# Optimization experiments

Measured on AMD Instinct MI355X. Metric: run time of the kernel, lower is better.

## Reference

```python
import jax, jax.numpy as jnp
import numpy as np
import math

B = 1024
FV = 4096
E = 256
Z = E + 1
EPS = 1e-3
INNER_NSTEP = 8
INNER_LR = 0.5
NS = 16


def setup_inputs() -> dict:
    key = jax.random.key(0)
    ks = jax.random.split(key, 6)
    img = jax.random.uniform(ks[0], (B, FV), dtype=jnp.float32)
    lab = jax.random.randint(ks[1], (B,), 0, 10, dtype=jnp.int64)
    w_dec_w = jax.random.normal(ks[2], (FV, E), dtype=jnp.float32) / np.sqrt(E)
    w_dec_b = jnp.zeros((FV,), dtype=jnp.float32)
    whz_w = jax.random.normal(ks[3], (E, Z), dtype=jnp.float32) / np.sqrt(Z)
    whz_b = jnp.zeros((E,), dtype=jnp.float32)
    b_loc_prior = jax.random.normal(ks[4], (Z,), dtype=jnp.float32) * 0.1
    b_scale_out = jnp.zeros((), dtype=jnp.float32)
    return {"img": img, "lab": lab, "w_dec_w": w_dec_w, "w_dec_b": w_dec_b,
            "whz_w": whz_w, "whz_b": whz_b, "b_loc_prior": b_loc_prior,
            "b_scale_out": b_scale_out}


def reference(img, lab, w_dec_w, w_dec_b, whz_w, whz_b, b_loc_prior, b_scale_out):
    del lab  # unused by loss_joint_lp
    img_flat = img.reshape((img.shape[0], -1))  # [B, FV]
    Bn = img_flat.shape[0]
    node_h = jnp.full((Bn, E), EPS, dtype=img.dtype)
    node_z = jnp.full((Bn, Z), EPS, dtype=img.dtype)
    out_prec = jnp.exp(2.0 * b_scale_out)
    log_prior_sig = jax.nn.log_sigmoid(b_loc_prior)  # [Z]

    def step(carry, k):
        node_h, node_z = carry
        k1, k2 = jax.random.split(k)
        node_e = node_h @ w_dec_w.T + w_dec_b                     # [B, FV]
        dh1 = ((img_flat - node_e) * out_prec) @ w_dec_w          # [B, E]
        h_post_log = node_z @ whz_w.T + whz_b                     # [B, E]
        dh2 = jax.nn.log_sigmoid(h_post_log)
        dz1 = (node_h * jax.nn.sigmoid(-h_post_log)) @ whz_w + log_prior_sig  # [B, Z]
        h_next = jax.nn.sigmoid(dh1 + dh2)
        z_next = jax.nn.sigmoid(dz1)
        sel_h = jax.random.uniform(k1, node_h.shape) < INNER_LR
        sel_z = jax.random.uniform(k2, node_z.shape) < INNER_LR
        node_h = jnp.where(sel_h, 0.5 * (node_h + h_next), node_h)
        node_z = jnp.where(sel_z, 0.5 * (node_z + z_next), node_z)
        node_h = jax.lax.stop_gradient(node_h)  # mirrors .detach()
        node_z = jax.lax.stop_gradient(node_z)
        return (node_h, node_z), None

    loop_keys = jax.random.split(jax.random.key(42), INNER_NSTEP)
    (node_h, node_z), _ = jax.lax.scan(step, (node_h, node_z), loop_keys)

    # Importance-weighted bound with NS Bernoulli samples
    sk = jax.random.split(jax.random.key(7), 2)
    z_noise = (jax.random.uniform(sk[0], (NS, Bn, Z)) < node_z).astype(img.dtype)
    h_post_log = z_noise @ whz_w.T + whz_b                        # [NS, B, E]
    h_noise = (jax.random.uniform(sk[1], (NS, Bn, E)) < jax.nn.sigmoid(h_post_log)).astype(img.dtype)
    loc = h_noise @ w_dec_w.T + w_dec_b                           # [NS, B, FV]

    # Normal(loc, exp(b_scale_out)).log_prob(img_flat)
    inv_scale = jnp.exp(-b_scale_out)
    lp_external = (-0.5 * ((img_flat - loc) * inv_scale) ** 2
                   - b_scale_out - 0.5 * math.log(2.0 * math.pi))  # [NS, B, FV]

    # Bernoulli(logits=b_loc_prior).log_prob - Bernoulli(probs=node_z).log_prob
    lp_prior = z_noise * b_loc_prior - jax.nn.softplus(b_loc_prior)
    lp_post = z_noise * jnp.log(node_z) + (1.0 - z_noise) * jnp.log1p(-node_z)
    lp_internal = lp_prior - lp_post                               # [NS, B, Z]

    joint = lp_internal.sum(-1) + lp_external.sum(-1)              # [NS, B]
    lse = jax.nn.logsumexp(joint, axis=0) - math.log(NS)           # [B]
    return -lse.mean(0)
```

## Files before the change

### kernel.cpp

```cpp
#include <hip/hip_runtime.h>
#include <stdint.h>

#define B_    1024
#define FV_   4096
#define E_    256
#define Z_    257
#define NS_   16
#define NSB_  16384
#define EPS_  1e-3f

typedef __attribute__((ext_vector_type(8))) short short8v;
typedef __attribute__((ext_vector_type(4))) float f32x4;
#define MFMA16(a,b,c) __builtin_amdgcn_mfma_f32_16x16x32_bf16(a,b,c,0,0,0)

__host__ __device__ __forceinline__ uint32_t rotl32(uint32_t v, int r){
  return (v << r) | (v >> (32 - r));
}
__host__ __device__ __forceinline__ void tf2x32(uint32_t k0, uint32_t k1,
    uint32_t x0, uint32_t x1, uint32_t* o0, uint32_t* o1){
  uint32_t ks2 = k0 ^ k1 ^ 0x1BD11BDAu;
  x0 += k0; x1 += k1;
#define TFR(r) { x0 += x1; x1 = rotl32(x1, (r)); x1 ^= x0; }
  TFR(13) TFR(15) TFR(26) TFR(6)
  x0 += k1;  x1 += ks2 + 1u;
  TFR(17) TFR(29) TFR(16) TFR(24)
  x0 += ks2; x1 += k0 + 2u;
  TFR(13) TFR(15) TFR(26) TFR(6)
  x0 += k0;  x1 += k1 + 3u;
  TFR(17) TFR(29) TFR(16) TFR(24)
  x0 += k1;  x1 += ks2 + 4u;
  TFR(13) TFR(15) TFR(26) TFR(6)
  x0 += ks2; x1 += k0 + 5u;
#undef TFR
  *o0 = x0; *o1 = x1;
}
__device__ __forceinline__ uint64_t tf64(uint32_t k0, uint32_t k1, uint32_t c){
  uint32_t a, b; tf2x32(k0, k1, 0u, c, &a, &b);
  return ((uint64_t)b << 32) | (uint64_t)a;
}
__device__ __forceinline__ float u01(uint32_t bits){
  return __uint_as_float((bits >> 9) | 0x3f800000u) - 1.0f;
}
__device__ __forceinline__ float logsigf(float x){
  return fminf(x, 0.f) - __logf(1.f + __expf(-fabsf(x)));
}
__device__ __forceinline__ float sigf(float x){ return 1.f / (1.f + __expf(-x)); }
__device__ __forceinline__ unsigned short f2bf(float f){
  uint32_t b = __float_as_uint(f);
  return (unsigned short)((b + 0x7fffu + ((b >> 16) & 1u)) >> 16);
}
__device__ __forceinline__ float bf2f(unsigned short u){
  return __uint_as_float(((uint32_t)u) << 16);
}

__global__ void k_prepw(const float* __restrict__ whz,
                        unsigned short* __restrict__ whzPh,
                        unsigned short* __restrict__ whzTPh){
  int r = blockIdx.x, t = threadIdx.x;
  if (r < 256){
    for (int z = t; z < 288; z += 256)
      whzPh[(size_t)r * 288 + z] = (z < Z_) ? f2bf(whz[(size_t)r * Z_ + z]) : (unsigned short)0;
  }
  whzTPh[(size_t)r * 256 + t] = (r < Z_) ? f2bf(whz[(size_t)t * Z_ + r]) : (unsigned short)0;
}

__global__ __launch_bounds__(256) void k_prepimg(const float* __restrict__ img,
    const float* __restrict__ wb, unsigned short* __restrict__ imgb,
    float* __restrict__ r2){
  int b = blockIdx.x, t = threadIdx.x;
  float s = 0.f;
#pragma unroll
  for (int i = 0; i < 4; i++){
    int col = t * 4 + i * 1024;
    float4 v = *(const float4*)&img[(size_t)b * FV_ + col];
    float4 wv = *(const float4*)&wb[col];
    float d0 = v.x - wv.x, d1 = v.y - wv.y, d2 = v.z - wv.z, d3 = v.w - wv.w;
    s = fmaf(d0, d0, fmaf(d1, d1, fmaf(d2, d2, fmaf(d3, d3, s))));
    ushort4 o; o.x = f2bf(d0); o.y = f2bf(d1); o.z = f2bf(d2); o.w = f2bf(d3);
    *(ushort4*)&imgb[(size_t)b * FV_ + col] = o;
  }
  __shared__ float red[256];
  red[t] = s; __syncthreads();
  for (int w = 128; w > 0; w >>= 1){ if (t < w) red[t] += red[t + w]; __syncthreads(); }
  if (!t) r2[b] = red[0];
}

__global__ void k_prepwt(const float* __restrict__ W, unsigned short* __restrict__ Wt){
  __shared__ float ld[32][33];
  int f0 = blockIdx.x * 32, e0 = blockIdx.y * 32;
  int t = threadIdx.x, tx = t & 31, ty = t >> 5;
#pragma unroll
  for (int sub = 0; sub < 4; sub++){
    int r = ty + 8 * sub;
    ld[r][tx] = W[(size_t)(f0 + r) * 256 + e0 + tx];
  }
  __syncthreads();
#pragma unroll
  for (int sub = 0; sub < 4; sub++){
    int r = ty + 8 * sub;
    Wt[(size_t)(e0 + r) * 4096 + f0 + tx] = f2bf(ld[tx][r]);
  }
}

__global__ __launch_bounds__(256) void k_ata_mfma(const unsigned short* __restrict__ Wt,
                                                  float* __restrict__ part){
  int t = threadIdx.x, lane = t & 63, w = t >> 6, l15 = lane & 15, l4 = lane >> 4;
  int m0 = blockIdx.x * 16;
  size_t kc = (size_t)blockIdx.y * 256;
  f32x4 acc[4];
#pragma unroll
  for (int q = 0; q < 4; q++) acc[q] = (f32x4){0.f, 0.f, 0.f, 0.f};
  for (int kt = 0; kt < 8; kt++){
    short8v a = *(const short8v*)&Wt[(size_t)(m0 + l15) * 4096 + kc + kt * 32 + l4 * 8];
#pragma unroll
    for (int q = 0; q < 4; q++){
      short8v b = *(const short8v*)&Wt[(size_t)(w * 64 + q * 16 + l15) * 4096 + kc + kt * 32 + l4 * 8];
      acc[q] = MFMA16(a, b, acc[q]);
    }
  }
  float* dst = part + (size_t)blockIdx.y * 65536;
#pragma unroll
  for (int q = 0; q < 4; q++)
#pragma unroll
    for (int j = 0; j < 4; j++)
      dst[(size_t)(m0 + l4 * 4 + j) * 256 + w * 64 + q * 16 + l15] = acc[q][j];
}

__global__ __launch_bounds__(256) void k_pp_mfma(const unsigned short* __restrict__ imgb,
                                                 const unsigned short* __restrict__ Wt,
                                                 float* __restrict__ part){
  int t = threadIdx.x, lane = t & 63, w = t >> 6, l15 = lane & 15, l4 = lane >> 4;
  int m0 = blockIdx.x * 32;
  size_t kc = (size_t)blockIdx.y * 512;
  f32x4 acc0[4], acc1[4];
#pragma unroll
  for (int q = 0; q < 4; q++){ acc0[q] = (f32x4){0.f,0.f,0.f,0.f}; acc1[q] = (f32x4){0.f,0.f,0.f,0.f}; }
  for (int kt = 0; kt < 16; kt++){
    short8v a0 = *(const short8v*)&imgb[(size_t)(m0 + l15) * 4096 + kc + kt * 32 + l4 * 8];
    short8v a1 = *(const short8v*)&imgb[(size_t)(m0 + 16 + l15) * 4096 + kc + kt * 32 + l4 * 8];
#pragma unroll
    for (int q = 0; q < 4; q++){
      short8v b = *(const short8v*)&Wt[(size_t)(w * 64 + q * 16 + l15) * 4096 + kc + kt * 32 + l4 * 8];
      acc0[q] = MFMA16(a0, b, acc0[q]);
      acc1[q] = MFMA16(a1, b, acc1[q]);
    }
  }
  float* dst = part + (size_t)blockIdx.y * (B_ * 256);
#pragma unroll
  for (int q = 0; q < 4; q++)
#pragma unroll
    for (int j = 0; j < 4; j++){
      dst[(size_t)(m0 + l4 * 4 + j) * 256 + w * 64 + q * 16 + l15] = acc0[q][j];
      dst[(size_t)(m0 + 16 + l4 * 4 + j) * 256 + w * 64 + q * 16 + l15] = acc1[q][j];
    }
}

template<int P, bool BF>
__global__ void k_reduceP(const float* __restrict__ src, float* __restrict__ dstF,
                          unsigned short* __restrict__ dstH, int n){
  int i = blockIdx.x * 256 + threadIdx.x;
  if (i >= n) return;
  float s = 0.f;
#pragma unroll
  for (int p = 0; p < P; p++) s += src[(size_t)p * n + i];
  if (BF) dstH[i] = f2bf(s); else dstF[i] = s;
}

__global__ __launch_bounds__(512, 1) void k_inner(
    const unsigned short* __restrict__ whzPh,
    const unsigned short* __restrict__ whzTPh,
    const unsigned short* __restrict__ Gh,
    const float* __restrict__ whzb,
    const float* __restrict__ blp,
    const float* __restrict__ Pp,
    const float* __restrict__ bso,
    float* __restrict__ nzOut, float* __restrict__ cA, float* __restrict__ rowB,
    uint32_t hk00, uint32_t hk01, uint32_t hk10, uint32_t hk11,
    uint32_t zk00, uint32_t zk01, uint32_t zk10, uint32_t zk11)
{
  __shared__ unsigned short zb[16][296];
  __shared__ unsigned short hbuf[2][16][296];
  __shared__ unsigned short sgb[16][296];
  __shared__ float zl[16][260];
  __shared__ float ppl[16][256];
  __shared__ float lsb[272];
  __shared__ float xbl[272];
  __shared__ float w256l[256];
  __shared__ uint64_t hbitL[272][2];
  __shared__ uint64_t zbitL[272][2];

  const int t = threadIdx.x;
  const int lane = t & 63;
  const int w = t >> 6;
  const int l15 = lane & 15;
  const int l4 = lane >> 4;
  const int blk = blockIdx.x;
  const int b0 = blk * 16;
  const int n0 = w * 32 + l15;
  const int n1 = n0 + 16;

  const unsigned short epsb = f2bf(EPS_);
  for (int i = t; i < 16 * 296; i += 512){
    int r = i / 296, c = i % 296;
    zb[r][c] = (c < Z_) ? epsb : (unsigned short)0;
    hbuf[0][r][c] = (c < 256) ? epsb : (unsigned short)0;
    hbuf[1][r][c] = 0;
    sgb[r][c] = 0;
  }
  for (int i = t; i < 16 * 260; i += 512){
    int r = i / 260, c = i % 260;
    zl[r][c] = (c < Z_) ? EPS_ : 0.f;
  }
  for (int i = t; i < 4096; i += 512)
    ppl[i >> 8][i & 255] = Pp[(size_t)(b0 + (i >> 8)) * 256 + (i & 255)];
  if (t < 272){
    float x = (t < Z_) ? blp[t] : 0.f;
    xbl[t] = x;
    lsb[t] = logsigf(x);
    hbitL[t][0] = tf64(hk00, hk01, (uint32_t)(blk * 272 + t));
    hbitL[t][1] = tf64(hk10, hk11, (uint32_t)(blk * 272 + t));
    zbitL[t][0] = tf64(zk00, zk01, (uint32_t)(blk * 272 + t));
    zbitL[t][1] = tf64(zk10, zk11, (uint32_t)(blk * 272 + t));
  }
  if (t < 256) w256l[t] = bf2f(whzTPh[(size_t)256 * 256 + t]);

  const unsigned short* wApt0 = &whzPh[(size_t)n0 * 288 + l4 * 8];
  const unsigned short* wApt1 = &whzPh[(size_t)n1 * 288 + l4 * 8];
  const unsigned short* wBpt0 = &Gh[(size_t)n0 * 256 + l4 * 8];
  const unsigned short* wBpt1 = &Gh[(size_t)n1 * 256 + l4 * 8];
  const unsigned short* wCpt0 = &whzTPh[(size_t)n0 * 256 + l4 * 8];
  const unsigned short* wCpt1 = &whzTPh[(size_t)n1 * 256 + l4 * 8];
  const float w256A0 = bf2f(whzPh[(size_t)n0 * 288 + 256]);
  const float w256A1 = bf2f(whzPh[(size_t)n1 * 288 + 256]);
  const float op = __expf(2.f * bso[0]);
  const float wbr0 = whzb[n0], wbr1 = whzb[n1];
  const float lsr0 = logsigf(blp[n0]), lsr1 = logsigf(blp[n1]);
  const float lsr2 = logsigf(blp[256]);
  float hreg0[4] = {EPS_, EPS_, EPS_, EPS_};
  float hreg1[4] = {EPS_, EPS_, EPS_, EPS_};
  __syncthreads();

  for (int s = 0; s < 8; s++){
    const int sg = s >> 2, sh = (s & 3) << 4;
    const int cur = s & 1, nx = cur ^ 1;

    f32x4 aA0 = {0.f, 0.f, 0.f, 0.f};
    {
      short8v wt[8];
#pragma unroll
      for (int kt = 0; kt < 8; kt++) wt[kt] = *(const short8v*)(wApt0 + kt * 32);
#pragma unroll
      for (int kt = 0; kt < 8; kt++)
        aA0 = MFMA16(*(const short8v*)&zb[l15][kt * 32 + l4 * 8], wt[kt], aA0);
    }
    f32x4 aA1 = {0.f, 0.f, 0.f, 0.f};
    {
      short8v wt[8];
#pragma unroll
      for (int kt = 0; kt < 8; kt++) wt[kt] = *(const short8v*)(wApt1 + kt * 32);
#pragma unroll
      for (int kt = 0; kt < 8; kt++)
        aA1 = MFMA16(*(const short8v*)&zb[l15][kt * 32 + l4 * 8], wt[kt], aA1);
    }
    float d2r0[4], d2r1[4];
#pragma unroll
    for (int j = 0; j < 4; j++){
      int m = l4 * 4 + j;
      float z256v = bf2f(zb[m][256]);
      float hpl0 = aA0[j] + wbr0 + z256v * w256A0;
      float hpl1 = aA1[j] + wbr1 + z256v * w256A1;
      d2r0[j] = logsigf(hpl0);
      d2r1[j] = logsigf(hpl1);
      sgb[m][n0] = f2bf(hreg0[j] * sigf(-hpl0));
      sgb[m][n1] = f2bf(hreg1[j] * sigf(-hpl1));
    }
    __syncthreads();

    f32x4 aB0 = {0.f, 0.f, 0.f, 0.f};
    {
      short8v wt[8];
#pragma unroll
      for (int kt = 0; kt < 8; kt++) wt[kt] = *(const short8v*)(wBpt0 + kt * 32);
#pragma unroll
      for (int kt = 0; kt < 8; kt++)
        aB0 = MFMA16(*(const short8v*)&hbuf[cur][l15][kt * 32 + l4 * 8], wt[kt], aB0);
    }
    f32x4 aB1 = {0.f, 0.f, 0.f, 0.f};
    {
      short8v wt[8];
#pragma unroll
      for (int kt = 0; kt < 8; kt++) wt[kt] = *(const short8v*)(wBpt1 + kt * 32);
#pragma unroll
      for (int kt = 0; kt < 8; kt++)
        aB1 = MFMA16(*(const short8v*)&hbuf[cur][l15][kt * 32 + l4 * 8], wt[kt], aB1);
    }
    f32x4 aC0 = {0.f, 0.f, 0.f, 0.f};
    {
      short8v wt[8];
#pragma unroll
      for (int kt = 0; kt < 8; kt++) wt[kt] = *(const short8v*)(wCpt0 + kt * 32);
#pragma unroll
      for (int kt = 0; kt < 8; kt++)
        aC0 = MFMA16(*(const short8v*)&sgb[l15][kt * 32 + l4 * 8], wt[kt], aC0);
    }
    f32x4 aC1 = {0.f, 0.f, 0.f, 0.f};
    {
      short8v wt[8];
#pragma unroll
      for (int kt = 0; kt < 8; kt++) wt[kt] = *(const short8v*)(wCpt1 + kt * 32);
#pragma unroll
      for (int kt = 0; kt < 8; kt++)
        aC1 = MFMA16(*(const short8v*)&sgb[l15][kt * 32 + l4 * 8], wt[kt], aC1);
    }
    float zdot = 0.f;
    if (w == 0){
      int r = lane & 15, kg = lane >> 4;
#pragma unroll
      for (int c = 0; c < 8; c++){
        short8v sv = *(const short8v*)&sgb[r][kg * 64 + c * 8];
#pragma unroll
        for (int i = 0; i < 8; i++)
          zdot = fmaf(bf2f((unsigned short)sv[i]), w256l[kg * 64 + c * 8 + i], zdot);
      }
      zdot += __shfl_xor(zdot, 16);
      zdot += __shfl_xor(zdot, 32);
    }

    {
      uint64_t hb0w = hbitL[n0][sg], hb1w = hbitL[n1][sg];
#pragma unroll
      for (int j = 0; j < 4; j++){
        int m = l4 * 4 + j;
        float hn0 = sigf(op * (ppl[m][n0] - aB0[j]) + d2r0[j]);
        float hn1 = sigf(op * (ppl[m][n1] - aB1[j]) + d2r1[j]);
        if ((hb0w >> (sh | m)) & 1ull) hreg0[j] = 0.5f * (hreg0[j] + hn0);
        if ((hb1w >> (sh | m)) & 1ull) hreg1[j] = 0.5f * (hreg1[j] + hn1);
        hbuf[nx][m][n0] = f2bf(hreg0[j]);
        hbuf[nx][m][n1] = f2bf(hreg1[j]);
      }
    }
    {
      uint64_t zb0w = zbitL[n0][sg], zb1w = zbitL[n1][sg];
#pragma unroll
      for (int j = 0; j < 4; j++){
        int m = l4 * 4 + j;
        float zx0 = sigf(aC0[j] + lsr0);
        float old0 = zl[m][n0];
        float nz0 = ((zb0w >> (sh | m)) & 1ull) ? 0.5f * (old0 + zx0) : old0;
        zl[m][n0] = nz0; zb[m][n0] = f2bf(nz0);
        float zx1 = sigf(aC1[j] + lsr1);
        float old1 = zl[m][n1];
        float nz1 = ((zb1w >> (sh | m)) & 1ull) ? 0.5f * (old1 + zx1) : old1;
        zl[m][n1] = nz1; zb[m][n1] = f2bf(nz1);
      }
    }
    if (w == 0 && lane < 16){
      int r = lane;
      uint64_t zw = zbitL[256][sg];
      float zx = sigf(zdot + lsr2);
      float old = zl[r][256];
      float nz = ((zw >> (sh | r)) & 1ull) ? 0.5f * (old + zx) : old;
      zl[r][256] = nz; zb[r][256] = f2bf(nz);
    }
    __syncthreads();
  }

  {
    int r = t >> 5, g = t & 31;
    float s = 0.f;
    for (int c = g; c < Z_; c += 32){
      float pz = zl[r][c];
      float lgp = __logf(pz);
      float lgq = log1pf(-pz);
      float x = xbl[c];
      nzOut[(size_t)(b0 + r) * Z_ + c] = pz;
      cA[(size_t)(b0 + r) * Z_ + c] = x - lgp + lgq;
      s += -(x - lsb[c]) - lgq;
    }
#pragma unroll
    for (int m = 16; m >= 1; m >>= 1) s += __shfl_xor(s, m);
    if (g == 0) rowB[b0 + r] = s;
  }
}

__global__ __launch_bounds__(128) void k_znoise(const float* __restrict__ nzF,
    const float* __restrict__ cA, const float* __restrict__ rowB,
    unsigned short* __restrict__ znb, float* __restrict__ lpint,
    uint32_t k0, uint32_t k1){
  int r = blockIdx.x, t = threadIdx.x;
  int b = r & (B_ - 1);
  float acc = 0.f;
  uint32_t o0, o1;
  tf2x32(k0, k1, 0u, (uint32_t)(r * 130 + t), &o0, &o1);
  int z0 = 2 * t, z1 = 2 * t + 1;
  {
    float pz = nzF[(size_t)b * Z_ + z0];
    int zv = u01(o0) < pz;
    znb[(size_t)r * 288 + z0] = zv ? (unsigned short)0x3F80 : (unsigned short)0;
    if (zv) acc += cA[(size_t)b * Z_ + z0];
  }
  {
    float pz = nzF[(size_t)b * Z_ + z1];
    int zv = u01(o1) < pz;
    znb[(size_t)r * 288 + z1] = zv ? (unsigned short)0x3F80 : (unsigned short)0;
    if (zv) acc += cA[(size_t)b * Z_ + z1];
  }
  if (t == 0){
    uint32_t p0, p1;
    tf2x32(k0, k1, 0u, (uint32_t)(r * 130 + 128), &p0, &p1);
    float pz = nzF[(size_t)b * Z_ + 256];
    int zv = u01(p0) < pz;
    znb[(size_t)r * 288 + 256] = zv ? (unsigned short)0x3F80 : (unsigned short)0;
    if (zv) acc += cA[(size_t)b * Z_ + 256];
  }
  if (t < 31) znb[(size_t)r * 288 + 257 + t] = 0;
  __shared__ float red[128];
  red[t] = acc; __syncthreads();
  for (int w = 64; w > 0; w >>= 1){ if (t < w) red[t] += red[t + w]; __syncthreads(); }
  if (!t) lpint[r] = rowB[b] + red[0];
}

__global__ __launch_bounds__(256) void k_gemm1(const unsigned short* __restrict__ znb,
    const unsigned short* __restrict__ whzPh, const float* __restrict__ whzb,
    unsigned short* __restrict__ hnb, uint32_t k0, uint32_t k1){
  int t = threadIdx.x, lane = t & 63, w = t >> 6, l15 = lane & 15, l4 = lane >> 4;
  int m0 = blockIdx.x * 32;
  short8v af0[9], af1[9];
#pragma unroll
  for (int kt = 0; kt < 9; kt++){
    af0[kt] = *(const short8v*)&znb[(size_t)(m0 + l15) * 288 + kt * 32 + l4 * 8];
    af1[kt] = *(const short8v*)&znb[(size_t)(m0 + 16 + l15) * 288 + kt * 32 + l4 * 8];
  }
#pragma unroll
  for (int q = 0; q < 4; q++){
    int n = w * 64 + q * 16 + l15;
    f32x4 acc0 = {0.f, 0.f, 0.f, 0.f}, acc1 = {0.f, 0.f, 0.f, 0.f};
#pragma unroll
    for (int kt = 0; kt < 9; kt++){
      short8v b = *(const short8v*)&whzPh[(size_t)n * 288 + kt * 32 + l4 * 8];
      acc0 = MFMA16(af0[kt], b, acc0);
      acc1 = MFMA16(af1[kt], b, acc1);
    }
    float wbv = whzb[n];
#pragma unroll
    for (int i = 0; i < 2; i++){
      int rowbase = m0 + i * 16 + l4 * 4;
      uint32_t c0 = (uint32_t)((rowbase >> 1) * 256 + n);
      uint32_t a0, b0, a1, b1;
      tf2x32(k0, k1, 0u, c0, &a0, &b0);
      tf2x32(k0, k1, 0u, c0 + 256, &a1, &b1);
      float u[4] = {u01(a0), u01(b0), u01(a1), u01(b1)};
      const f32x4& ac = i ? acc1 : acc0;
#pragma unroll
      for (int j = 0; j < 4; j++){
        float pr = sigf(ac[j] + wbv);
        hnb[(size_t)(rowbase + j) * 256 + n] = (u[j] < pr) ? (unsigned short)0x3F80 : (unsigned short)0;
      }
    }
  }
}

__global__ __launch_bounds__(256) void k_gemm2(const unsigned short* __restrict__ hnb,
    const unsigned short* __restrict__ Gh, const float* __restrict__ Pp,
    const float* __restrict__ r2, const float* __restrict__ lpint,
    const float* __restrict__ bso, float* __restrict__ joint){
  int t = threadIdx.x, lane = t & 63, w = t >> 6, l15 = lane & 15, l4 = lane >> 4;
  int m0 = blockIdx.x * 32;
  short8v af0[8], af1[8];
#pragma unroll
  for (int kt = 0; kt < 8; kt++){
    af0[kt] = *(const short8v*)&hnb[(size_t)(m0 + l15) * 256 + kt * 32 + l4 * 8];
    af1[kt] = *(const short8v*)&hnb[(size_t)(m0 + 16 + l15) * 256 + kt * 32 + l4 * 8];
  }
  float s1a[4] = {0.f,0.f,0.f,0.f}, s2a[4] = {0.f,0.f,0.f,0.f};
  float s1b[4] = {0.f,0.f,0.f,0.f}, s2b[4] = {0.f,0.f,0.f,0.f};
#pragma unroll
  for (int q = 0; q < 4; q++){
    int n = w * 64 + q * 16 + l15;
    f32x4 acc0 = {0.f, 0.f, 0.f, 0.f}, acc1 = {0.f, 0.f, 0.f, 0.f};
#pragma unroll
    for (int kt = 0; kt < 8; kt++){
      short8v b = *(const short8v*)&Gh[(size_t)n * 256 + kt * 32 + l4 * 8];
      acc0 = MFMA16(af0[kt], b, acc0);
      acc1 = MFMA16(af1[kt], b, acc1);
    }
#pragma unroll
    for (int j = 0; j < 4; j++){
      int gm0 = m0 + l4 * 4 + j, gm1 = gm0 + 16;
      float hv0 = bf2f(hnb[(size_t)gm0 * 256 + n]);
      float hv1 = bf2f(hnb[(size_t)gm1 * 256 + n]);
      float pp0 = Pp[(size_t)(gm0 & (B_ - 1)) * 256 + n];
      float pp1 = Pp[(size_t)(gm1 & (B_ - 1)) * 256 + n];
      s1a[j] = fmaf(hv0, acc0[j], s1a[j]);
      s2a[j] = fmaf(hv0, pp0, s2a[j]);
      s1b[j] = fmaf(hv1, acc1[j], s1b[j]);
      s2b[j] = fmaf(hv1, pp1, s2b[j]);
    }
  }
#pragma unroll
  for (int j = 0; j < 4; j++){
#pragma unroll
    for (int msk = 1; msk < 16; msk <<= 1){
      s1a[j] += __shfl_xor(s1a[j], msk);
      s2a[j] += __shfl_xor(s2a[j], msk);
      s1b[j] += __shfl_xor(s1b[j], msk);
      s2b[j] += __shfl_xor(s2b[j], msk);
    }
  }
  __shared__ float sred[4][32][2];
  if (l15 == 0){
#pragma unroll
    for (int j = 0; j < 4; j++){
      sred[w][l4 * 4 + j][0] = s1a[j];
      sred[w][l4 * 4 + j][1] = s2a[j];
      sred[w][16 + l4 * 4 + j][0] = s1b[j];
      sred[w][16 + l4 * 4 + j][1] = s2b[j];
    }
  }
  __syncthreads();
  if (t < 32){
    float S1 = 0.f, S2 = 0.f;
#pragma unroll
    for (int wv = 0; wv < 4; wv++){ S1 += sred[wv][t][0]; S2 += sred[wv][t][1]; }
    int gm = m0 + t;
    int b = gm & (B_ - 1);
    float bs = bso[0];
    float isc2 = __expf(-2.f * bs);
    float se = r2[b] - 2.f * S2 + S1;
    joint[gm] = lpint[gm] - 0.5f * isc2 * se - (float)FV_ * (bs + 0.91893853320467274f);
  }
}

__global__ __launch_bounds__(1024) void k_final(const float* __restrict__ joint, float* __restrict__ out){
  int b = threadIdx.x;
  float mx = -3.0e38f;
  for (int n = 0; n < NS_; n++) mx = fmaxf(mx, joint[(size_t)n * B_ + b]);
  float s = 0.f;
  for (int n = 0; n < NS_; n++) s += __expf(joint[(size_t)n * B_ + b] - mx);
  float lse = mx + __logf(s) - 2.772588722239781f;
  __shared__ float red[1024];
  red[b] = lse; __syncthreads();
  for (int w = 512; w > 0; w >>= 1){ if (b < w) red[b] += red[b + w]; __syncthreads(); }
  if (!b) out[0] = -red[0] / (float)B_;
}

extern "C" void kernel_launch(void* const* d_in, const int* in_sizes, int n_in,
                              void* d_out, int out_size, void* d_ws, size_t ws_size,
                              hipStream_t stream){
  const float* img  = (const float*)d_in[0];
  const float* W    = (const float*)d_in[2];
  const float* wb   = (const float*)d_in[3];
  const float* whz  = (const float*)d_in[4];
  const float* whzb = (const float*)d_in[5];
  const float* blp  = (const float*)d_in[6];
  const float* bso  = (const float*)d_in[7];
  float* out = (float*)d_out;
  float* ws = (float*)d_ws;
  (void)in_sizes; (void)n_in; (void)out_size; (void)ws_size;

  size_t off = 0;
  auto nxt = [&](size_t n){ size_t o = off; off += (n + 63) & ~(size_t)63; return o; };
  float* Pp    = ws + nxt((size_t)B_ * 256);
  float* r2    = ws + nxt(B_);
  float* lpint = ws + nxt(NSB_);
  float* joint = ws + nxt(NSB_);
  float* nzF   = ws + nxt((size_t)B_ * Z_);
  float* cA    = ws + nxt((size_t)B_ * Z_);
  float* rowB  = ws + nxt(B_);
  unsigned short* Gh     = (unsigned short*)(ws + nxt((size_t)256 * 256 / 2));
  unsigned short* whzPh  = (unsigned short*)(ws + nxt((size_t)256 * 288 / 2));
  unsigned short* whzTPh = (unsigned short*)(ws + nxt((size_t)272 * 256 / 2));
  unsigned short* Wt     = (unsigned short*)(ws + nxt((size_t)256 * 4096 / 2));
  unsigned short* imgb   = (unsigned short*)(ws + nxt((size_t)B_ * FV_ / 2));
  float* znRgn = ws + nxt((size_t)NSB_ * 288 / 2);
  float* hnRgn = ws + nxt((size_t)NSB_ * 256 / 2);

  unsigned short* znb = (unsigned short*)znRgn;
  unsigned short* hnb = (unsigned short*)hnRgn;
  float* ataPart = znRgn;
  float* ppPart  = hnRgn;

  uint32_t hk00, hk01, hk10, hk11, zk00, zk01, zk10, zk11;
  tf2x32(0u, 42u, 1u, 0u, &hk00, &hk01);
  tf2x32(0u, 42u, 1u, 1u, &hk10, &hk11);
  tf2x32(0u, 42u, 2u, 0u, &zk00, &zk01);
  tf2x32(0u, 42u, 2u, 1u, &zk10, &zk11);
  uint32_t sk00, sk01, sk10, sk11;
  tf2x32(0u, 7u, 0u, 0u, &sk00, &sk01);
  tf2x32(0u, 7u, 0u, 1u, &sk10, &sk11);

  k_prepimg<<<dim3(B_), 256, 0, stream>>>(img, wb, imgb, r2);
  k_prepwt<<<dim3(128, 8), 256, 0, stream>>>(W, Wt);
  k_prepw<<<dim3(272), 256, 0, stream>>>(whz, whzPh, whzTPh);
  k_ata_mfma<<<dim3(16, 16), 256, 0, stream>>>(Wt, ataPart);
  k_reduceP<16, true><<<dim3(256), 256, 0, stream>>>(ataPart, nullptr, Gh, 65536);
  k_pp_mfma<<<dim3(32, 8), 256, 0, stream>>>(imgb, Wt, ppPart);
  k_reduceP<8, false><<<dim3(1024), 256, 0, stream>>>(ppPart, Pp, nullptr, B_ * 256);

  k_inner<<<dim3(64), 512, 0, stream>>>(whzPh, whzTPh, Gh, whzb, blp, Pp, bso,
                                        nzF, cA, rowB,
                                        hk00, hk01, hk10, hk11, zk00, zk01, zk10, zk11);

  k_znoise<<<dim3(NSB_), 128, 0, stream>>>(nzF, cA, rowB, znb, lpint, sk00, sk01);
  k_gemm1<<<dim3(512), 256, 0, stream>>>(znb, whzPh, whzb, hnb, sk10, sk11);
  k_gemm2<<<dim3(512), 256, 0, stream>>>(hnb, Gh, Pp, r2, lpint, bso, joint);
  k_final<<<dim3(1), 1024, 0, stream>>>(joint, out);
}
```

Measured before the change: 150.6 us.

## Merge prep, GEMM and reduce launches and fuse sampling stage into one kernel

The three prep kernels become one block-indexed kernel, the two partial GEMMs share one launch, and the two reductions share another, which cuts the launch count. The z-noise sampling, the z→h GEMM with h sampling, and the Gram-matrix GEMM are fused into a single k_phase2 kernel. That kernel keeps the z and h bit matrices in shared memory instead of writing them to global and reading them back. In exchange, each block runs its sampling loop serially, and the partial buffers now get their own workspace regions instead of aliasing.

Measured after the change: 133.9 us. 11.1% less time.

```diff
diff --git a/kernel.cpp b/kernel.cpp
--- a/kernel.cpp
+++ b/kernel.cpp
@@ -53,117 +53,125 @@
   return __uint_as_float(((uint32_t)u) << 16);
 }
 
-__global__ void k_prepw(const float* __restrict__ whz,
-                        unsigned short* __restrict__ whzPh,
-                        unsigned short* __restrict__ whzTPh){
-  int r = blockIdx.x, t = threadIdx.x;
-  if (r < 256){
-    for (int z = t; z < 288; z += 256)
-      whzPh[(size_t)r * 288 + z] = (z < Z_) ? f2bf(whz[(size_t)r * Z_ + z]) : (unsigned short)0;
-  }
-  whzTPh[(size_t)r * 256 + t] = (r < Z_) ? f2bf(whz[(size_t)t * Z_ + r]) : (unsigned short)0;
-}
-
-__global__ __launch_bounds__(256) void k_prepimg(const float* __restrict__ img,
-    const float* __restrict__ wb, unsigned short* __restrict__ imgb,
-    float* __restrict__ r2){
-  int b = blockIdx.x, t = threadIdx.x;
-  float s = 0.f;
-#pragma unroll
-  for (int i = 0; i < 4; i++){
-    int col = t * 4 + i * 1024;
-    float4 v = *(const float4*)&img[(size_t)b * FV_ + col];
-    float4 wv = *(const float4*)&wb[col];
-    float d0 = v.x - wv.x, d1 = v.y - wv.y, d2 = v.z - wv.z, d3 = v.w - wv.w;
-    s = fmaf(d0, d0, fmaf(d1, d1, fmaf(d2, d2, fmaf(d3, d3, s))));
-    ushort4 o; o.x = f2bf(d0); o.y = f2bf(d1); o.z = f2bf(d2); o.w = f2bf(d3);
-    *(ushort4*)&imgb[(size_t)b * FV_ + col] = o;
-  }
+__global__ __launch_bounds__(256) void k_prep(
+    const float* __restrict__ img, const float* __restrict__ wb,
+    unsigned short* __restrict__ imgb, float* __restrict__ r2,
+    const float* __restrict__ W, unsigned short* __restrict__ Wt,
+    const float* __restrict__ whz, unsigned short* __restrict__ whzPh,
+    unsigned short* __restrict__ whzTPh){
+  __shared__ float ld[32][33];
   __shared__ float red[256];
-  red[t] = s; __syncthreads();
-  for (int w = 128; w > 0; w >>= 1){ if (t < w) red[t] += red[t + w]; __syncthreads(); }
-  if (!t) r2[b] = red[0];
-}
-
-__global__ void k_prepwt(const float* __restrict__ W, unsigned short* __restrict__ Wt){
-  __shared__ float ld[32][33];
-  int f0 = blockIdx.x * 32, e0 = blockIdx.y * 32;
-  int t = threadIdx.x, tx = t & 31, ty = t >> 5;
-#pragma unroll
-  for (int sub = 0; sub < 4; sub++){
-    int r = ty + 8 * sub;
-    ld[r][tx] = W[(size_t)(f0 + r) * 256 + e0 + tx];
-  }
-  __syncthreads();
-#pragma unroll
-  for (int sub = 0; sub < 4; sub++){
-    int r = ty + 8 * sub;
-    Wt[(size_t)(e0 + r) * 4096 + f0 + tx] = f2bf(ld[tx][r]);
-  }
-}
-
-__global__ __launch_bounds__(256) void k_ata_mfma(const unsigned short* __restrict__ Wt,
-                                                  float* __restrict__ part){
+  int bid = blockIdx.x, t = threadIdx.x;
+  if (bid < 1024){
+    int b = bid;
+    float s = 0.f;
+#pragma unroll
+    for (int i = 0; i < 4; i++){
+      int col = t * 4 + i * 1024;
+      float4 v = *(const float4*)&img[(size_t)b * FV_ + col];
+      float4 wv = *(const float4*)&wb[col];
+      float d0 = v.x - wv.x, d1 = v.y - wv.y, d2 = v.z - wv.z, d3 = v.w - wv.w;
+      s = fmaf(d0, d0, fmaf(d1, d1, fmaf(d2, d2, fmaf(d3, d3, s))));
+      ushort4 o; o.x = f2bf(d0); o.y = f2bf(d1); o.z = f2bf(d2); o.w = f2bf(d3);
+      *(ushort4*)&imgb[(size_t)b * FV_ + col] = o;
+    }
+    red[t] = s; __syncthreads();
+    for (int w = 128; w > 0; w >>= 1){ if (t < w) red[t] += red[t + w]; __syncthreads(); }
+    if (!t) r2[b] = red[0];
+  } else if (bid < 2048){
+    int idx = bid - 1024;
+    int f0 = (idx & 127) * 32, e0 = (idx >> 7) * 32;
+    int tx = t & 31, ty = t >> 5;
+#pragma unroll
+    for (int sub = 0; sub < 4; sub++){
+      int r = ty + 8 * sub;
+      ld[r][tx] = W[(size_t)(f0 + r) * 256 + e0 + tx];
+    }
+    __syncthreads();
+#pragma unroll
+    for (int sub = 0; sub < 4; sub++){
+      int r = ty + 8 * sub;
+      Wt[(size_t)(e0 + r) * 4096 + f0 + tx] = f2bf(ld[tx][r]);
+    }
+  } else {
+    int r = bid - 2048;
+    if (r < 256){
+      for (int z = t; z < 288; z += 256)
+        whzPh[(size_t)r * 288 + z] = (z < Z_) ? f2bf(whz[(size_t)r * Z_ + z]) : (unsigned short)0;
+    }
+    whzTPh[(size_t)r * 256 + t] = (r < Z_) ? f2bf(whz[(size_t)t * Z_ + r]) : (unsigned short)0;
+  }
+}
+
+__global__ __launch_bounds__(256) void k_gemms(const unsigned short* __restrict__ Wt,
+    const unsigned short* __restrict__ imgb,
+    float* __restrict__ ataPart, float* __restrict__ ppPart){
+  int bid = blockIdx.x;
   int t = threadIdx.x, lane = t & 63, w = t >> 6, l15 = lane & 15, l4 = lane >> 4;
-  int m0 = blockIdx.x * 16;
-  size_t kc = (size_t)blockIdx.y * 256;
-  f32x4 acc[4];
-#pragma unroll
-  for (int q = 0; q < 4; q++) acc[q] = (f32x4){0.f, 0.f, 0.f, 0.f};
-  for (int kt = 0; kt < 8; kt++){
-    short8v a = *(const short8v*)&Wt[(size_t)(m0 + l15) * 4096 + kc + kt * 32 + l4 * 8];
-#pragma unroll
-    for (int q = 0; q < 4; q++){
-      short8v b = *(const short8v*)&Wt[(size_t)(w * 64 + q * 16 + l15) * 4096 + kc + kt * 32 + l4 * 8];
-      acc[q] = MFMA16(a, b, acc[q]);
-    }
-  }
-  float* dst = part + (size_t)blockIdx.y * 65536;
-#pragma unroll
-  for (int q = 0; q < 4; q++)
-#pragma unroll
-    for (int j = 0; j < 4; j++)
-      dst[(size_t)(m0 + l4 * 4 + j) * 256 + w * 64 + q * 16 + l15] = acc[q][j];
-}
-
-__global__ __launch_bounds__(256) void k_pp_mfma(const unsigned short* __restrict__ imgb,
-                                                 const unsigned short* __restrict__ Wt,
-                                                 float* __restrict__ part){
-  int t = threadIdx.x, lane = t & 63, w = t >> 6, l15 = lane & 15, l4 = lane >> 4;
-  int m0 = blockIdx.x * 32;
-  size_t kc = (size_t)blockIdx.y * 512;
-  f32x4 acc0[4], acc1[4];
-#pragma unroll
-  for (int q = 0; q < 4; q++){ acc0[q] = (f32x4){0.f,0.f,0.f,0.f}; acc1[q] = (f32x4){0.f,0.f,0.f,0.f}; }
-  for (int kt = 0; kt < 16; kt++){
-    short8v a0 = *(const short8v*)&imgb[(size_t)(m0 + l15) * 4096 + kc + kt * 32 + l4 * 8];
-    short8v a1 = *(const short8v*)&imgb[(size_t)(m0 + 16 + l15) * 4096 + kc + kt * 32 + l4 * 8];
-#pragma unroll
-    for (int q = 0; q < 4; q++){
-      short8v b = *(const short8v*)&Wt[(size_t)(w * 64 + q * 16 + l15) * 4096 + kc + kt * 32 + l4 * 8];
-      acc0[q] = MFMA16(a0, b, acc0[q]);
-      acc1[q] = MFMA16(a1, b, acc1[q]);
-    }
-  }
-  float* dst = part + (size_t)blockIdx.y * (B_ * 256);
-#pragma unroll
-  for (int q = 0; q < 4; q++)
-#pragma unroll
-    for (int j = 0; j < 4; j++){
-      dst[(size_t)(m0 + l4 * 4 + j) * 256 + w * 64 + q * 16 + l15] = acc0[q][j];
-      dst[(size_t)(m0 + 16 + l4 * 4 + j) * 256 + w * 64 + q * 16 + l15] = acc1[q][j];
-    }
-}
-
-template<int P, bool BF>
-__global__ void k_reduceP(const float* __restrict__ src, float* __restrict__ dstF,
-                          unsigned short* __restrict__ dstH, int n){
-  int i = blockIdx.x * 256 + threadIdx.x;
-  if (i >= n) return;
-  float s = 0.f;
-#pragma unroll
-  for (int p = 0; p < P; p++) s += src[(size_t)p * n + i];
-  if (BF) dstH[i] = f2bf(s); else dstF[i] = s;
+  if (bid < 256){
+    int m0 = (bid & 15) * 16;
+    size_t kc = (size_t)(bid >> 4) * 256;
+    f32x4 acc[4];
+#pragma unroll
+    for (int q = 0; q < 4; q++) acc[q] = (f32x4){0.f, 0.f, 0.f, 0.f};
+    for (int kt = 0; kt < 8; kt++){
+      short8v a = *(const short8v*)&Wt[(size_t)(m0 + l15) * 4096 + kc + kt * 32 + l4 * 8];
+#pragma unroll
+      for (int q = 0; q < 4; q++){
+        short8v b = *(const short8v*)&Wt[(size_t)(w * 64 + q * 16 + l15) * 4096 + kc + kt * 32 + l4 * 8];
+        acc[q] = MFMA16(a, b, acc[q]);
+      }
+    }
+    float* dst = ataPart + (size_t)(bid >> 4) * 65536;
+#pragma unroll
+    for (int q = 0; q < 4; q++)
+#pragma unroll
+      for (int j = 0; j < 4; j++)
+        dst[(size_t)(m0 + l4 * 4 + j) * 256 + w * 64 + q * 16 + l15] = acc[q][j];
+  } else {
+    int idx = bid - 256;
+    int m0 = (idx & 31) * 32;
+    size_t kc = (size_t)(idx >> 5) * 512;
+    f32x4 acc0[4], acc1[4];
+#pragma unroll
+    for (int q = 0; q < 4; q++){ acc0[q] = (f32x4){0.f,0.f,0.f,0.f}; acc1[q] = (f32x4){0.f,0.f,0.f,0.f}; }
+    for (int kt = 0; kt < 16; kt++){
+      short8v a0 = *(const short8v*)&imgb[(size_t)(m0 + l15) * 4096 + kc + kt * 32 + l4 * 8];
+      short8v a1 = *(const short8v*)&imgb[(size_t)(m0 + 16 + l15) * 4096 + kc + kt * 32 + l4 * 8];
+#pragma unroll
+      for (int q = 0; q < 4; q++){
+        short8v b = *(const short8v*)&Wt[(size_t)(w * 64 + q * 16 + l15) * 4096 + kc + kt * 32 + l4 * 8];
+        acc0[q] = MFMA16(a0, b, acc0[q]);
+        acc1[q] = MFMA16(a1, b, acc1[q]);
+      }
+    }
+    float* dst = ppPart + (size_t)(idx >> 5) * (B_ * 256);
+#pragma unroll
+    for (int q = 0; q < 4; q++)
+#pragma unroll
+      for (int j = 0; j < 4; j++){
+        dst[(size_t)(m0 + l4 * 4 + j) * 256 + w * 64 + q * 16 + l15] = acc0[q][j];
+        dst[(size_t)(m0 + 16 + l4 * 4 + j) * 256 + w * 64 + q * 16 + l15] = acc1[q][j];
+      }
+  }
+}
+
+__global__ void k_reduce(const float* __restrict__ ataPart, unsigned short* __restrict__ Gh,
+                         const float* __restrict__ ppPart, float* __restrict__ Pp){
+  int bid = blockIdx.x, t = threadIdx.x;
+  if (bid < 256){
+    int i = bid * 256 + t;
+    float s = 0.f;
+#pragma unroll
+    for (int p = 0; p < 16; p++) s += ataPart[(size_t)p * 65536 + i];
+    Gh[i] = f2bf(s);
+  } else {
+    int i = (bid - 256) * 256 + t;
+    float s = 0.f;
+#pragma unroll
+    for (int p = 0; p < 8; p++) s += ppPart[(size_t)p * (B_ * 256) + i];
+    Pp[i] = s;
+  }
 }
 
 __global__ __launch_bounds__(512, 1) void k_inner(
@@ -383,151 +391,164 @@
   }
 }
 
-__global__ __launch_bounds__(128) void k_znoise(const float* __restrict__ nzF,
-    const float* __restrict__ cA, const float* __restrict__ rowB,
-    unsigned short* __restrict__ znb, float* __restrict__ lpint,
-    uint32_t k0, uint32_t k1){
-  int r = blockIdx.x, t = threadIdx.x;
-  int b = r & (B_ - 1);
-  float acc = 0.f;
-  uint32_t o0, o1;
-  tf2x32(k0, k1, 0u, (uint32_t)(r * 130 + t), &o0, &o1);
-  int z0 = 2 * t, z1 = 2 * t + 1;
+__global__ __launch_bounds__(256) void k_phase2(
+    const float* __restrict__ nzF, const float* __restrict__ cA,
+    const float* __restrict__ rowBg,
+    const unsigned short* __restrict__ whzPh, const float* __restrict__ whzb,
+    const unsigned short* __restrict__ Gh, const float* __restrict__ Pp,
+    const float* __restrict__ r2, const float* __restrict__ bso,
+    float* __restrict__ joint,
+    uint32_t zk0, uint32_t zk1, uint32_t hk0, uint32_t hk1){
+  __shared__ unsigned short znl[32][296];
+  __shared__ unsigned short hnl[32][264];
+  __shared__ float lpl[32];
+  __shared__ float sred[4][32][2];
+
+  const int t = threadIdx.x, lane = t & 63, w = t >> 6;
+  const int l15 = lane & 15, l4 = lane >> 4;
+  const int m0 = blockIdx.x * 32;
+  const int bb0 = m0 & (B_ - 1);
+
+  for (int i = t; i < 32 * 32; i += 256){
+    znl[i >> 5][256 + (i & 31)] = 0;
+  }
+  if (t < 32) lpl[t] = rowBg[bb0 + t];
+  __syncthreads();
+
+  for (int sub = 0; sub < 16; sub++){
+    int rl = sub * 2 + (t >> 7);
+    int rg = m0 + rl;
+    int b = bb0 + rl;
+    int tpos = t & 127;
+    uint32_t o0, o1;
+    tf2x32(zk0, zk1, 0u, (uint32_t)(rg * 130 + tpos), &o0, &o1);
+    int z0 = 2 * tpos;
+    float acc = 0.f;
+    {
+      float pz0 = nzF[(size_t)b * Z_ + z0];
+      float pz1 = nzF[(size_t)b * Z_ + z0 + 1];
+      int v0 = u01(o0) < pz0;
+      int v1 = u01(o1) < pz1;
+      uint32_t pack = (v0 ? 0x3F80u : 0u) | (v1 ? 0x3F800000u : 0u);
+      *(uint32_t*)&znl[rl][z0] = pack;
+      if (v0) acc += cA[(size_t)b * Z_ + z0];
+      if (v1) acc += cA[(size_t)b * Z_ + z0 + 1];
+    }
+    if (tpos == 0){
+      uint32_t p0, p1;
+      tf2x32(zk0, zk1, 0u, (uint32_t)(rg * 130 + 128), &p0, &p1);
+      float pz = nzF[(size_t)b * Z_ + 256];
+      int v = u01(p0) < pz;
+      znl[rl][256] = v ? (unsigned short)0x3F80 : (unsigned short)0;
+      if (v) acc += cA[(size_t)b * Z_ + 256];
+    }
+#pragma unroll
+    for (int m = 32; m >= 1; m >>= 1) acc += __shfl_xor(acc, m);
+    if (lane == 0) atomicAdd(&lpl[rl], acc);
+  }
+  __syncthreads();
+
   {
-    float pz = nzF[(size_t)b * Z_ + z0];
-    int zv = u01(o0) < pz;
-    znb[(size_t)r * 288 + z0] = zv ? (unsigned short)0x3F80 : (unsigned short)0;
-    if (zv) acc += cA[(size_t)b * Z_ + z0];
-  }
+    short8v af0[9], af1[9];
+#pragma unroll
+    for (int kt = 0; kt < 9; kt++){
+      af0[kt] = *(const short8v*)&znl[l15][kt * 32 + l4 * 8];
+      af1[kt] = *(const short8v*)&znl[16 + l15][kt * 32 + l4 * 8];
+    }
+#pragma unroll
+    for (int q = 0; q < 4; q++){
+      int n = w * 64 + q * 16 + l15;
+      f32x4 acc0 = {0.f,0.f,0.f,0.f}, acc1 = {0.f,0.f,0.f,0.f};
+#pragma unroll
+      for (int kt = 0; kt < 9; kt++){
+        short8v bfr = *(const short8v*)&whzPh[(size_t)n * 288 + kt * 32 + l4 * 8];
+        acc0 = MFMA16(af0[kt], bfr, acc0);
+        acc1 = MFMA16(af1[kt], bfr, acc1);
+      }
+      float wbv = whzb[n];
+#pragma unroll
+      for (int i = 0; i < 2; i++){
+        int rbl = i * 16 + l4 * 4;
+        int rbg = m0 + rbl;
+        uint32_t c0 = (uint32_t)((rbg >> 1) * 256 + n);
+        uint32_t ra0, rb0, ra1, rb1;
+        tf2x32(hk0, hk1, 0u, c0, &ra0, &rb0);
+        tf2x32(hk0, hk1, 0u, c0 + 256, &ra1, &rb1);
+        float u[4] = {u01(ra0), u01(rb0), u01(ra1), u01(rb1)};
+        const f32x4& ac = i ? acc1 : acc0;
+#pragma unroll
+        for (int j = 0; j < 4; j++){
+          float pr = sigf(ac[j] + wbv);
+          hnl[rbl + j][n] = (u[j] < pr) ? (unsigned short)0x3F80 : (unsigned short)0;
+        }
+      }
+    }
+  }
+  __syncthreads();
+
   {
-    float pz = nzF[(size_t)b * Z_ + z1];
-    int zv = u01(o1) < pz;
-    znb[(size_t)r * 288 + z1] = zv ? (unsigned short)0x3F80 : (unsigned short)0;
-    if (zv) acc += cA[(size_t)b * Z_ + z1];
-  }
-  if (t == 0){
-    uint32_t p0, p1;
-    tf2x32(k0, k1, 0u, (uint32_t)(r * 130 + 128), &p0, &p1);
-    float pz = nzF[(size_t)b * Z_ + 256];
-    int zv = u01(p0) < pz;
-    znb[(size_t)r * 288 + 256] = zv ? (unsigned short)0x3F80 : (unsigned short)0;
-    if (zv) acc += cA[(size_t)b * Z_ + 256];
-  }
-  if (t < 31) znb[(size_t)r * 288 + 257 + t] = 0;
-  __shared__ float red[128];
-  red[t] = acc; __syncthreads();
-  for (int w = 64; w > 0; w >>= 1){ if (t < w) red[t] += red[t + w]; __syncthreads(); }
-  if (!t) lpint[r] = rowB[b] + red[0];
-}
-
-__global__ __launch_bounds__(256) void k_gemm1(const unsigned short* __restrict__ znb,
-    const unsigned short* __restrict__ whzPh, const float* __restrict__ whzb,
-    unsigned short* __restrict__ hnb, uint32_t k0, uint32_t k1){
-  int t = threadIdx.x, lane = t & 63, w = t >> 6, l15 = lane & 15, l4 = lane >> 4;
-  int m0 = blockIdx.x * 32;
-  short8v af0[9], af1[9];
-#pragma unroll
-  for (int kt = 0; kt < 9; kt++){
-    af0[kt] = *(const short8v*)&znb[(size_t)(m0 + l15) * 288 + kt * 32 + l4 * 8];
-    af1[kt] = *(const short8v*)&znb[(size_t)(m0 + 16 + l15) * 288 + kt * 32 + l4 * 8];
-  }
-#pragma unroll
-  for (int q = 0; q < 4; q++){
-    int n = w * 64 + q * 16 + l15;
-    f32x4 acc0 = {0.f, 0.f, 0.f, 0.f}, acc1 = {0.f, 0.f, 0.f, 0.f};
-#pragma unroll
-    for (int kt = 0; kt < 9; kt++){
-      short8v b = *(const short8v*)&whzPh[(size_t)n * 288 + kt * 32 + l4 * 8];
-      acc0 = MFMA16(af0[kt], b, acc0);
-      acc1 = MFMA16(af1[kt], b, acc1);
-    }
-    float wbv = whzb[n];
-#pragma unroll
-    for (int i = 0; i < 2; i++){
-      int rowbase = m0 + i * 16 + l4 * 4;
-      uint32_t c0 = (uint32_t)((rowbase >> 1) * 256 + n);
-      uint32_t a0, b0, a1, b1;
-      tf2x32(k0, k1, 0u, c0, &a0, &b0);
-      tf2x32(k0, k1, 0u, c0 + 256, &a1, &b1);
-      float u[4] = {u01(a0), u01(b0), u01(a1), u01(b1)};
-      const f32x4& ac = i ? acc1 : acc0;
+    short8v bf0[8], bf1[8];
+#pragma unroll
+    for (int kt = 0; kt < 8; kt++){
+      bf0[kt] = *(const short8v*)&hnl[l15][kt * 32 + l4 * 8];
+      bf1[kt] = *(const short8v*)&hnl[16 + l15][kt * 32 + l4 * 8];
+    }
+    float s1a[4]={0.f,0.f,0.f,0.f}, s2a[4]={0.f,0.f,0.f,0.f};
+    float s1b[4]={0.f,0.f,0.f,0.f}, s2b[4]={0.f,0.f,0.f,0.f};
+#pragma unroll
+    for (int q = 0; q < 4; q++){
+      int n = w * 64 + q * 16 + l15;
+      f32x4 acc0 = {0.f,0.f,0.f,0.f}, acc1 = {0.f,0.f,0.f,0.f};
+#pragma unroll
+      for (int kt = 0; kt < 8; kt++){
+        short8v bfr = *(const short8v*)&Gh[(size_t)n * 256 + kt * 32 + l4 * 8];
+        acc0 = MFMA16(bf0[kt], bfr, acc0);
+        acc1 = MFMA16(bf1[kt], bfr, acc1);
+      }
 #pragma unroll
       for (int j = 0; j < 4; j++){
-        float pr = sigf(ac[j] + wbv);
-        hnb[(size_t)(rowbase + j) * 256 + n] = (u[j] < pr) ? (unsigned short)0x3F80 : (unsigned short)0;
-      }
-    }
-  }
-}
-
-__global__ __launch_bounds__(256) void k_gemm2(const unsigned short* __restrict__ hnb,
-    const unsigned short* __restrict__ Gh, const float* __restrict__ Pp,
-    const float* __restrict__ r2, const float* __restrict__ lpint,
-    const float* __restrict__ bso, float* __restrict__ joint){
-  int t = threadIdx.x, lane = t & 63, w = t >> 6, l15 = lane & 15, l4 = lane >> 4;
-  int m0 = blockIdx.x * 32;
-  short8v af0[8], af1[8];
-#pragma unroll
-  for (int kt = 0; kt < 8; kt++){
-    af0[kt] = *(const short8v*)&hnb[(size_t)(m0 + l15) * 256 + kt * 32 + l4 * 8];
-    af1[kt] = *(const short8v*)&hnb[(size_t)(m0 + 16 + l15) * 256 + kt * 32 + l4 * 8];
-  }
-  float s1a[4] = {0.f,0.f,0.f,0.f}, s2a[4] = {0.f,0.f,0.f,0.f};
-  float s1b[4] = {0.f,0.f,0.f,0.f}, s2b[4] = {0.f,0.f,0.f,0.f};
-#pragma unroll
-  for (int q = 0; q < 4; q++){
-    int n = w * 64 + q * 16 + l15;
-    f32x4 acc0 = {0.f, 0.f, 0.f, 0.f}, acc1 = {0.f, 0.f, 0.f, 0.f};
-#pragma unroll
-    for (int kt = 0; kt < 8; kt++){
-      short8v b = *(const short8v*)&Gh[(size_t)n * 256 + kt * 32 + l4 * 8];
-      acc0 = MFMA16(af0[kt], b, acc0);
-      acc1 = MFMA16(af1[kt], b, acc1);
+        int gl0 = l4 * 4 + j, gl1 = gl0 + 16;
+        float hv0 = bf2f(hnl[gl0][n]);
+        float hv1 = bf2f(hnl[gl1][n]);
+        float pp0 = Pp[(size_t)((m0 + gl0) & (B_ - 1)) * 256 + n];
+        float pp1 = Pp[(size_t)((m0 + gl1) & (B_ - 1)) * 256 + n];
+        s1a[j] = fmaf(hv0, acc0[j], s1a[j]);
+        s2a[j] = fmaf(hv0, pp0, s2a[j]);
+        s1b[j] = fmaf(hv1, acc1[j], s1b[j]);
+        s2b[j] = fmaf(hv1, pp1, s2b[j]);
+      }
     }
 #pragma unroll
     for (int j = 0; j < 4; j++){
-      int gm0 = m0 + l4 * 4 + j, gm1 = gm0 + 16;
-      float hv0 = bf2f(hnb[(size_t)gm0 * 256 + n]);
-      float hv1 = bf2f(hnb[(size_t)gm1 * 256 + n]);
-      float pp0 = Pp[(size_t)(gm0 & (B_ - 1)) * 256 + n];
-      float pp1 = Pp[(size_t)(gm1 & (B_ - 1)) * 256 + n];
-      s1a[j] = fmaf(hv0, acc0[j], s1a[j]);
-      s2a[j] = fmaf(hv0, pp0, s2a[j]);
-      s1b[j] = fmaf(hv1, acc1[j], s1b[j]);
-      s2b[j] = fmaf(hv1, pp1, s2b[j]);
-    }
-  }
-#pragma unroll
-  for (int j = 0; j < 4; j++){
-#pragma unroll
-    for (int msk = 1; msk < 16; msk <<= 1){
-      s1a[j] += __shfl_xor(s1a[j], msk);
-      s2a[j] += __shfl_xor(s2a[j], msk);
-      s1b[j] += __shfl_xor(s1b[j], msk);
-      s2b[j] += __shfl_xor(s2b[j], msk);
-    }
-  }
-  __shared__ float sred[4][32][2];
-  if (l15 == 0){
-#pragma unroll
-    for (int j = 0; j < 4; j++){
-      sred[w][l4 * 4 + j][0] = s1a[j];
-      sred[w][l4 * 4 + j][1] = s2a[j];
-      sred[w][16 + l4 * 4 + j][0] = s1b[j];
-      sred[w][16 + l4 * 4 + j][1] = s2b[j];
-    }
-  }
-  __syncthreads();
-  if (t < 32){
-    float S1 = 0.f, S2 = 0.f;
-#pragma unroll
-    for (int wv = 0; wv < 4; wv++){ S1 += sred[wv][t][0]; S2 += sred[wv][t][1]; }
-    int gm = m0 + t;
-    int b = gm & (B_ - 1);
-    float bs = bso[0];
-    float isc2 = __expf(-2.f * bs);
-    float se = r2[b] - 2.f * S2 + S1;
-    joint[gm] = lpint[gm] - 0.5f * isc2 * se - (float)FV_ * (bs + 0.91893853320467274f);
+#pragma unroll
+      for (int msk = 1; msk < 16; msk <<= 1){
+        s1a[j] += __shfl_xor(s1a[j], msk);
+        s2a[j] += __shfl_xor(s2a[j], msk);
+        s1b[j] += __shfl_xor(s1b[j], msk);
+        s2b[j] += __shfl_xor(s2b[j], msk);
+      }
+    }
+    if (l15 == 0){
+#pragma unroll
+      for (int j = 0; j < 4; j++){
+        sred[w][l4 * 4 + j][0] = s1a[j];
+        sred[w][l4 * 4 + j][1] = s2a[j];
+        sred[w][16 + l4 * 4 + j][0] = s1b[j];
+        sred[w][16 + l4 * 4 + j][1] = s2b[j];
+      }
+    }
+    __syncthreads();
+    if (t < 32){
+      float S1 = 0.f, S2 = 0.f;
+#pragma unroll
+      for (int wv = 0; wv < 4; wv++){ S1 += sred[wv][t][0]; S2 += sred[wv][t][1]; }
+      int gm = m0 + t;
+      int b = gm & (B_ - 1);
+      float bs = bso[0];
+      float isc2 = __expf(-2.f * bs);
+      float se = r2[b] - 2.f * S2 + S1;
+      joint[gm] = lpl[t] - 0.5f * isc2 * se - (float)FV_ * (bs + 0.91893853320467274f);
+    }
   }
 }
 
@@ -562,7 +583,6 @@
   auto nxt = [&](size_t n){ size_t o = off; off += (n + 63) & ~(size_t)63; return o; };
   float* Pp    = ws + nxt((size_t)B_ * 256);
   float* r2    = ws + nxt(B_);
-  float* lpint = ws + nxt(NSB_);
   float* joint = ws + nxt(NSB_);
   float* nzF   = ws + nxt((size_t)B_ * Z_);
   float* cA    = ws + nxt((size_t)B_ * Z_);
@@ -572,13 +592,8 @@
   unsigned short* whzTPh = (unsigned short*)(ws + nxt((size_t)272 * 256 / 2));
   unsigned short* Wt     = (unsigned short*)(ws + nxt((size_t)256 * 4096 / 2));
   unsigned short* imgb   = (unsigned short*)(ws + nxt((size_t)B_ * FV_ / 2));
-  float* znRgn = ws + nxt((size_t)NSB_ * 288 / 2);
-  float* hnRgn = ws + nxt((size_t)NSB_ * 256 / 2);
-
-  unsigned short* znb = (unsigned short*)znRgn;
-  unsigned short* hnb = (unsigned short*)hnRgn;
-  float* ataPart = znRgn;
-  float* ppPart  = hnRgn;
+  float* ataPart = ws + nxt((size_t)16 * 65536);
+  float* ppPart  = ws + nxt((size_t)8 * B_ * 256);
 
   uint32_t hk00, hk01, hk10, hk11, zk00, zk01, zk10, zk11;
   tf2x32(0u, 42u, 1u, 0u, &hk00, &hk01);
@@ -589,20 +604,13 @@
   tf2x32(0u, 7u, 0u, 0u, &sk00, &sk01);
   tf2x32(0u, 7u, 0u, 1u, &sk10, &sk11);
 
-  k_prepimg<<<dim3(B_), 256, 0, stream>>>(img, wb, imgb, r2);
-  k_prepwt<<<dim3(128, 8), 256, 0, stream>>>(W, Wt);
-  k_prepw<<<dim3(272), 256, 0, stream>>>(whz, whzPh, whzTPh);
-  k_ata_mfma<<<dim3(16, 16), 256, 0, stream>>>(Wt, ataPart);
-  k_reduceP<16, true><<<dim3(256), 256, 0, stream>>>(ataPart, nullptr, Gh, 65536);
-  k_pp_mfma<<<dim3(32, 8), 256, 0, stream>>>(imgb, Wt, ppPart);
-  k_reduceP<8, false><<<dim3(1024), 256, 0, stream>>>(ppPart, Pp, nullptr, B_ * 256);
-
+  k_prep<<<dim3(2320), 256, 0, stream>>>(img, wb, imgb, r2, W, Wt, whz, whzPh, whzTPh);
+  k_gemms<<<dim3(512), 256, 0, stream>>>(Wt, imgb, ataPart, ppPart);
+  k_reduce<<<dim3(1280), 256, 0, stream>>>(ataPart, Gh, ppPart, Pp);
   k_inner<<<dim3(64), 512, 0, stream>>>(whzPh, whzTPh, Gh, whzb, blp, Pp, bso,
                                         nzF, cA, rowB,
                                         hk00, hk01, hk10, hk11, zk00, zk01, zk10, zk11);
-
-  k_znoise<<<dim3(NSB_), 128, 0, stream>>>(nzF, cA, rowB, znb, lpint, sk00, sk01);
-  k_gemm1<<<dim3(512), 256, 0, stream>>>(znb, whzPh, whzb, hnb, sk10, sk11);
-  k_gemm2<<<dim3(512), 256, 0, stream>>>(hnb, Gh, Pp, r2, lpint, bso, joint);
+  k_phase2<<<dim3(512), 256, 0, stream>>>(nzF, cA, rowB, whzPh, whzb, Gh, Pp, r2, bso,
+                                          joint, sk00, sk01, sk10, sk11);
   k_final<<<dim3(1), 1024, 0, stream>>>(joint, out);
 }
```
